# Kernel optimization log

Measured on AMD Instinct MI355X. Metric: run time of the kernel, lower is better.

The kernel has to match this reference:

```python
import jax, jax.numpy as jnp
import numpy as np

N_NODES = 50000
IN_F = 256
OUT_F = 128
N_EDGES = 800000

def setup_inputs() -> dict:
    key = jax.random.key(0)
    k1, k2, k3, k4, k5 = jax.random.split(key, 5)
    x = jax.random.normal(k1, (N_NODES, IN_F), dtype=jnp.float32)
    # xavier_uniform on [in, out]
    limit = float(np.sqrt(6.0 / (IN_F + OUT_F)))
    weight = jax.random.uniform(k2, (IN_F, OUT_F), dtype=jnp.float32, minval=-limit, maxval=limit)
    adj_vals = jax.random.uniform(k3, (N_EDGES,), dtype=jnp.float32)
    adj_rows = jax.random.randint(k4, (N_EDGES,), 0, N_NODES, dtype=jnp.int32)
    adj_cols = jax.random.randint(k5, (N_EDGES,), 0, N_NODES, dtype=jnp.int32)
    return {"x": x, "weight": weight, "adj_vals": adj_vals, "adj_rows": adj_rows, "adj_cols": adj_cols}

def reference(x, weight, adj_vals, adj_rows, adj_cols):
    # dropout p=0.0 (eval) is identity
    support = x @ weight                      # [N, out]
    msgs = adj_vals[:, None] * support[adj_cols]  # [E, out] gather + scale
    output = jax.ops.segment_sum(msgs, adj_rows, num_segments=N_NODES)  # spmm
    return jax.nn.relu(output)
```

## Files before the change

### kernel.cpp

```cpp
#include <hip/hip_runtime.h>
#include <hip/hip_bf16.h>


#define IN_F  256
#define OUT_F 128
#define NPART 8

#define BM 64
#define BK 32
#define KP 40

typedef __attribute__((ext_vector_type(8))) short s16x8;
typedef __attribute__((ext_vector_type(4))) float f32x4;

static __device__ __forceinline__ unsigned short f2bf(float f) {
    union { float f; unsigned u; } v; v.f = f;
    unsigned r = v.u + 0x7FFFu + ((v.u >> 16) & 1u);
    return (unsigned short)(r >> 16);
}
static __device__ __forceinline__ float bf2f(unsigned short b) {
    union { unsigned u; float f; } v; v.u = ((unsigned)b) << 16;
    return v.f;
}

__global__ __launch_bounds__(256) void gcn_wsplit_kernel(
    const float* __restrict__ w, unsigned short* __restrict__ wh_T,
    unsigned short* __restrict__ wl_T)
{
    int cell = blockIdx.x * 256 + threadIdx.x;
    int c  = cell & (OUT_F - 1);
    int kq = cell >> 7;
    unsigned short h[4], l[4];
#pragma unroll
    for (int d = 0; d < 4; ++d) {
        float f = w[(size_t)(kq * 4 + d) * OUT_F + c];
        h[d] = f2bf(f);
        l[d] = f2bf(f - bf2f(h[d]));
    }
    *reinterpret_cast<ushort4*>(&wh_T[(size_t)c * IN_F + kq * 4]) =
        make_ushort4(h[0], h[1], h[2], h[3]);
    *reinterpret_cast<ushort4*>(&wl_T[(size_t)c * IN_F + kq * 4]) =
        make_ushort4(l[0], l[1], l[2], l[3]);
}

__global__ __launch_bounds__(256) void gcn_gemm_mfma_kernel(
    const float* __restrict__ x,
    const unsigned short* __restrict__ wh_T,
    const unsigned short* __restrict__ wl_T,
    unsigned short* __restrict__ support_bf, int n_nodes)
{
    __shared__ unsigned short xh_lds[BM][KP];
    __shared__ unsigned short xl_lds[BM][KP];
    __shared__ unsigned short wh_lds[OUT_F][KP];
    __shared__ unsigned short wl_lds[OUT_F][KP];

    const int tid  = threadIdx.x;
    const int lane = tid & 63;
    const int wid  = tid >> 6;
    const int wm   = (wid >> 1) * 32;
    const int wn   = (wid & 1) * 64;
    const int row0 = blockIdx.x * BM;

    const int lr = lane & 15;
    const int lg = lane >> 4;

    f32x4 acc[2][4];
#pragma unroll
    for (int st = 0; st < 2; ++st)
#pragma unroll
        for (int nt = 0; nt < 4; ++nt)
            acc[st][nt] = (f32x4){0.f, 0.f, 0.f, 0.f};

    for (int k0 = 0; k0 < IN_F; k0 += BK) {
        if (k0 > 0) __syncthreads();

#pragma unroll
        for (int i = 0; i < 2; ++i) {
            int cell = i * 256 + tid;
            int r    = cell >> 3;
            int kq   = cell & 7;
            int row  = row0 + r;
            float4 xv = make_float4(0.f, 0.f, 0.f, 0.f);
            if (row < n_nodes)
                xv = *reinterpret_cast<const float4*>(
                    &x[(size_t)row * IN_F + k0 + kq * 4]);
            unsigned short h0 = f2bf(xv.x), h1 = f2bf(xv.y),
                           h2 = f2bf(xv.z), h3 = f2bf(xv.w);
            *reinterpret_cast<ushort4*>(&xh_lds[r][kq * 4]) =
                make_ushort4(h0, h1, h2, h3);
            *reinterpret_cast<ushort4*>(&xl_lds[r][kq * 4]) =
                make_ushort4(f2bf(xv.x - bf2f(h0)), f2bf(xv.y - bf2f(h1)),
                             f2bf(xv.z - bf2f(h2)), f2bf(xv.w - bf2f(h3)));
        }
#pragma unroll
        for (int i = 0; i < 2; ++i) {
            int cell = i * 256 + tid;
            int c    = cell >> 2;
            int p    = cell & 3;
            s16x8 hv = *reinterpret_cast<const s16x8*>(
                &wh_T[(size_t)c * IN_F + k0 + p * 8]);
            s16x8 lv = *reinterpret_cast<const s16x8*>(
                &wl_T[(size_t)c * IN_F + k0 + p * 8]);
            *reinterpret_cast<s16x8*>(&wh_lds[c][p * 8]) = hv;
            *reinterpret_cast<s16x8*>(&wl_lds[c][p * 8]) = lv;
        }
        __syncthreads();

        s16x8 ah[2], al[2], bh[4], bl[4];
#pragma unroll
        for (int st = 0; st < 2; ++st) {
            int m = wm + st * 16 + lr;
            ah[st] = *reinterpret_cast<const s16x8*>(&xh_lds[m][lg * 8]);
            al[st] = *reinterpret_cast<const s16x8*>(&xl_lds[m][lg * 8]);
        }
#pragma unroll
        for (int nt = 0; nt < 4; ++nt) {
            int c = wn + nt * 16 + lr;
            bh[nt] = *reinterpret_cast<const s16x8*>(&wh_lds[c][lg * 8]);
            bl[nt] = *reinterpret_cast<const s16x8*>(&wl_lds[c][lg * 8]);
        }

#pragma unroll
        for (int st = 0; st < 2; ++st)
#pragma unroll
            for (int nt = 0; nt < 4; ++nt) {
                acc[st][nt] = __builtin_amdgcn_mfma_f32_16x16x32_bf16(
                    ah[st], bh[nt], acc[st][nt], 0, 0, 0);
                acc[st][nt] = __builtin_amdgcn_mfma_f32_16x16x32_bf16(
                    al[st], bh[nt], acc[st][nt], 0, 0, 0);
                acc[st][nt] = __builtin_amdgcn_mfma_f32_16x16x32_bf16(
                    ah[st], bl[nt], acc[st][nt], 0, 0, 0);
            }
    }

#pragma unroll
    for (int st = 0; st < 2; ++st) {
#pragma unroll
        for (int nt = 0; nt < 4; ++nt) {
#pragma unroll
            for (int r = 0; r < 4; ++r) {
                int m = row0 + wm + st * 16 + lg * 4 + r;
                int n = wn + nt * 16 + lr;
                if (m < n_nodes)
                    support_bf[(size_t)m * OUT_F + n] = f2bf(acc[st][nt][r]);
            }
        }
    }
}

#define VBK 32
#define XPAD 68
__global__ __launch_bounds__(256) void gcn_gemm_valu_kernel(
    const float* __restrict__ x, const float* __restrict__ w,
    float* __restrict__ support, int n_nodes)
{
    __shared__ float xs_t[VBK][XPAD];
    __shared__ float ws_[VBK][OUT_F];

    const int tid  = threadIdx.x;
    const int cg   = tid & 31;
    const int rg   = tid >> 5;
    const int row0 = blockIdx.x * BM;

    float acc[8][4];
#pragma unroll
    for (int i = 0; i < 8; ++i)
#pragma unroll
        for (int j = 0; j < 4; ++j) acc[i][j] = 0.f;

    for (int k0 = 0; k0 < IN_F; k0 += VBK) {
        if (k0 > 0) __syncthreads();
#pragma unroll
        for (int i = 0; i < 2; ++i) {
            int t   = tid + i * 256;
            int r   = t >> 3;
            int kk  = (t & 7) << 2;
            int row = row0 + r;
            float4 v = make_float4(0.f, 0.f, 0.f, 0.f);
            if (row < n_nodes)
                v = *reinterpret_cast<const float4*>(&x[(size_t)row * IN_F + k0 + kk]);
            xs_t[kk + 0][r] = v.x;
            xs_t[kk + 1][r] = v.y;
            xs_t[kk + 2][r] = v.z;
            xs_t[kk + 3][r] = v.w;
        }
#pragma unroll
        for (int i = 0; i < 4; ++i) {
            int fi = tid + i * 256;
            int kk = fi >> 5;
            int cc = (fi & 31) << 2;
            *reinterpret_cast<float4*>(&ws_[kk][cc]) =
                *reinterpret_cast<const float4*>(&w[(size_t)(k0 + kk) * OUT_F + cc]);
        }
        __syncthreads();
#pragma unroll
        for (int kk = 0; kk < VBK; ++kk) {
            float4 a0 = *reinterpret_cast<const float4*>(&xs_t[kk][rg * 4]);
            float4 a1 = *reinterpret_cast<const float4*>(&xs_t[kk][rg * 4 + 32]);
            float4 b  = *reinterpret_cast<const float4*>(&ws_[kk][cg * 4]);
            const float av[8] = {a0.x, a0.y, a0.z, a0.w, a1.x, a1.y, a1.z, a1.w};
            const float bv[4] = {b.x, b.y, b.z, b.w};
#pragma unroll
            for (int i = 0; i < 8; ++i)
#pragma unroll
                for (int j = 0; j < 4; ++j)
                    acc[i][j] += av[i] * bv[j];
        }
    }
#pragma unroll
    for (int i = 0; i < 8; ++i) {
        int row = row0 + rg * 4 + (i & 3) + (i >> 2) * 32;
        if (row < n_nodes) {
            float4 o = make_float4(acc[i][0], acc[i][1], acc[i][2], acc[i][3]);
            *reinterpret_cast<float4*>(&support[(size_t)row * OUT_F + cg * 4]) = o;
        }
    }
}

__global__ __launch_bounds__(256) void gcn_hist_kernel(
    const int* __restrict__ rows, int* __restrict__ deg,
    int n_edges, int node_pp)
{
    int part = blockIdx.x & 7;
    int e = (blockIdx.x >> 3) * 256 + threadIdx.x;
    if (e >= n_edges) return;
    int r = rows[e];
    if (r / node_pp != part) return;
    atomicAdd(&deg[r], 1);
}

__global__ __launch_bounds__(256) void gcn_scan1_kernel(
    const int* __restrict__ deg, int* __restrict__ offsets,
    int* __restrict__ block_sums, int n)
{
    __shared__ int part[256];
    const int tid  = threadIdx.x;
    const int base = blockIdx.x * 2048 + tid * 8;

    int v[8];
#pragma unroll
    for (int q = 0; q < 8; ++q) v[q] = 0;
    if (base + 7 < n) {
        int4 a = *reinterpret_cast<const int4*>(&deg[base]);
        int4 b = *reinterpret_cast<const int4*>(&deg[base + 4]);
        v[0] = a.x; v[1] = a.y; v[2] = a.z; v[3] = a.w;
        v[4] = b.x; v[5] = b.y; v[6] = b.z; v[7] = b.w;
    } else {
#pragma unroll
        for (int q = 0; q < 8; ++q)
            if (base + q < n) v[q] = deg[base + q];
    }
    int s = 0;
#pragma unroll
    for (int q = 0; q < 8; ++q) s += v[q];
    part[tid] = s;
    __syncthreads();
    for (int d = 1; d < 256; d <<= 1) {
        int t = (tid >= d) ? part[tid - d] : 0;
        __syncthreads();
        part[tid] += t;
        __syncthreads();
    }
    int run = part[tid] - s;
    int o[8];
#pragma unroll
    for (int q = 0; q < 8; ++q) { o[q] = run; run += v[q]; }
    if (base + 7 < n) {
        *reinterpret_cast<int4*>(&offsets[base])     = make_int4(o[0], o[1], o[2], o[3]);
        *reinterpret_cast<int4*>(&offsets[base + 4]) = make_int4(o[4], o[5], o[6], o[7]);
    } else {
#pragma unroll
        for (int q = 0; q < 8; ++q)
            if (base + q < n) offsets[base + q] = o[q];
    }
    if (tid == 255) block_sums[blockIdx.x] = part[255];
}

__global__ __launch_bounds__(256) void gcn_scan2_kernel(
    int* __restrict__ block_sums, int nb)
{
    __shared__ int part[256];
    const int tid = threadIdx.x;
    int s = (tid < nb) ? block_sums[tid] : 0;
    part[tid] = s;
    __syncthreads();
    for (int d = 1; d < 256; d <<= 1) {
        int t = (tid >= d) ? part[tid - d] : 0;
        __syncthreads();
        part[tid] += t;
        __syncthreads();
    }
    if (tid < nb) block_sums[tid] = part[tid] - s;
}

__global__ __launch_bounds__(256) void gcn_scan3_kernel(
    int* __restrict__ offsets, const int* __restrict__ block_sums, int n)
{
    const int base = blockIdx.x * 2048 + threadIdx.x * 8;
    const int add  = block_sums[blockIdx.x];
    if (base + 7 < n) {
        int4 a = *reinterpret_cast<const int4*>(&offsets[base]);
        int4 b = *reinterpret_cast<const int4*>(&offsets[base + 4]);
        a.x += add; a.y += add; a.z += add; a.w += add;
        b.x += add; b.y += add; b.z += add; b.w += add;
        *reinterpret_cast<int4*>(&offsets[base])     = a;
        *reinterpret_cast<int4*>(&offsets[base + 4]) = b;
    } else {
#pragma unroll
        for (int q = 0; q < 8; ++q)
            if (base + q < n) offsets[base + q] += add;
    }
}

__global__ __launch_bounds__(256) void gcn_fill_kernel(
    const int* __restrict__ rows, const int* __restrict__ cols,
    const float* __restrict__ vals, int* __restrict__ offsets,
    unsigned int* __restrict__ csr_cv, int n_edges, int node_pp)
{
    int part = blockIdx.x & 7;
    int e = (blockIdx.x >> 3) * 256 + threadIdx.x;
    if (e >= n_edges) return;
    int r = rows[e];
    if (r / node_pp != part) return;
    int pos = atomicAdd(&offsets[r], 1);
    unsigned int cv = ((unsigned int)f2bf(vals[e]) << 16) | (unsigned int)cols[e];
    csr_cv[pos] = cv;
}

__global__ __launch_bounds__(256) void gcn_gather_kernel(
    const unsigned short* __restrict__ support_bf,
    const int* __restrict__ offsets,
    const unsigned int* __restrict__ csr_cv,
    float* __restrict__ out, int n_nodes)
{
    const int node = blockIdx.x * 4 + (threadIdx.x >> 6);
    const int lane = threadIdx.x & 63;
    if (node >= n_nodes) return;

    const int end   = offsets[node];
    const int start = (node == 0) ? 0 : offsets[node - 1];

    float2 acc = make_float2(0.f, 0.f);
    int j = start;
    for (; j + 7 < end; j += 8) {
        unsigned int cv[8];
        ushort2 s[8];
#pragma unroll
        for (int q = 0; q < 8; ++q) cv[q] = csr_cv[j + q];
#pragma unroll
        for (int q = 0; q < 8; ++q)
            s[q] = *reinterpret_cast<const ushort2*>(
                &support_bf[(size_t)(cv[q] & 0xFFFFu) * OUT_F + lane * 2]);
#pragma unroll
        for (int q = 0; q < 8; ++q) {
            float v = bf2f((unsigned short)(cv[q] >> 16));
            acc.x += v * bf2f(s[q].x);
            acc.y += v * bf2f(s[q].y);
        }
    }
    for (; j + 1 < end; j += 2) {
        unsigned int cv0 = csr_cv[j];
        unsigned int cv1 = csr_cv[j + 1];
        ushort2 s0 = *reinterpret_cast<const ushort2*>(
            &support_bf[(size_t)(cv0 & 0xFFFFu) * OUT_F + lane * 2]);
        ushort2 s1 = *reinterpret_cast<const ushort2*>(
            &support_bf[(size_t)(cv1 & 0xFFFFu) * OUT_F + lane * 2]);
        float v0 = bf2f((unsigned short)(cv0 >> 16));
        float v1 = bf2f((unsigned short)(cv1 >> 16));
        acc.x += v0 * bf2f(s0.x) + v1 * bf2f(s1.x);
        acc.y += v0 * bf2f(s0.y) + v1 * bf2f(s1.y);
    }
    if (j < end) {
        unsigned int cv0 = csr_cv[j];
        ushort2 s0 = *reinterpret_cast<const ushort2*>(
            &support_bf[(size_t)(cv0 & 0xFFFFu) * OUT_F + lane * 2]);
        float v0 = bf2f((unsigned short)(cv0 >> 16));
        acc.x += v0 * bf2f(s0.x);
        acc.y += v0 * bf2f(s0.y);
    }

    float2 o;
    o.x = fmaxf(acc.x, 0.f);
    o.y = fmaxf(acc.y, 0.f);
    *reinterpret_cast<float2*>(&out[(size_t)node * OUT_F + lane * 2]) = o;
}

__global__ __launch_bounds__(256) void gcn_scatter_kernel(
    const float* __restrict__ support, const float* __restrict__ vals,
    const int* __restrict__ rows, const int* __restrict__ cols,
    float* __restrict__ out, int n_edges)
{
    long long idx   = (long long)blockIdx.x * blockDim.x + threadIdx.x;
    long long total = (long long)n_edges * (OUT_F / 4);
    if (idx >= total) return;

    int e  = (int)(idx >> 5);
    int f4 = (int)(idx & 31);
    int r  = rows[e];
    int c  = cols[e];
    float v = vals[e];

    float4 s = *reinterpret_cast<const float4*>(&support[(size_t)c * OUT_F + f4 * 4]);
    float* o = &out[(size_t)r * OUT_F + f4 * 4];
    atomicAdd(o + 0, v * s.x);
    atomicAdd(o + 1, v * s.y);
    atomicAdd(o + 2, v * s.z);
    atomicAdd(o + 3, v * s.w);
}

__global__ __launch_bounds__(256) void gcn_relu_kernel(float* __restrict__ out, int n4)
{
    int idx = blockIdx.x * blockDim.x + threadIdx.x;
    if (idx >= n4) return;
    float4* p = reinterpret_cast<float4*>(out) + idx;
    float4 v = *p;
    v.x = fmaxf(v.x, 0.f);
    v.y = fmaxf(v.y, 0.f);
    v.z = fmaxf(v.z, 0.f);
    v.w = fmaxf(v.w, 0.f);
    *p = v;
}

static inline char* align16(char* p) {
    return (char*)(((uintptr_t)p + 15) & ~(uintptr_t)15);
}

extern "C" void kernel_launch(void* const* d_in, const int* in_sizes, int n_in,
                              void* d_out, int out_size, void* d_ws, size_t ws_size,
                              hipStream_t stream)
{
    const float* x    = (const float*)d_in[0];
    const float* w    = (const float*)d_in[1];
    const float* vals = (const float*)d_in[2];
    const int*   rows = (const int*)d_in[3];
    const int*   cols = (const int*)d_in[4];
    float* out = (float*)d_out;

    const int n_nodes = in_sizes[0] / IN_F;
    const int n_edges = in_sizes[2];

    const int scan_blocks = (n_nodes + 2047) / 2048;
    const int node_pp     = (n_nodes + NPART - 1) / NPART;

    char* p = (char*)d_ws;
    char*           supp_raw = p;                 p = align16(p + (size_t)n_nodes * OUT_F * sizeof(float));
    unsigned short* wh_T    = (unsigned short*)p; p = align16(p + (size_t)OUT_F * IN_F * sizeof(short));
    unsigned short* wl_T    = (unsigned short*)p; p = align16(p + (size_t)OUT_F * IN_F * sizeof(short));
    int*            offsets = (int*)p;            p = align16(p + (size_t)n_nodes * sizeof(int));
    int*            deg     = (int*)p;            p = align16(p + (size_t)n_nodes * sizeof(int));
    int*            bsums   = (int*)p;            p = align16(p + (size_t)256 * sizeof(int));
    unsigned int*   csr_cv  = (unsigned int*)p;   p = align16(p + (size_t)n_edges * sizeof(unsigned int));
    size_t needed = (size_t)(p - (char*)d_ws);

    const int gemm_blocks = (n_nodes + BM - 1) / BM;
    const int eb = (n_edges + 255) / 256;

    if (ws_size >= needed && scan_blocks <= 256 && n_nodes <= 65536) {
        unsigned short* support_bf = (unsigned short*)supp_raw;
        gcn_wsplit_kernel<<<(OUT_F * IN_F / 4) / 256, 256, 0, stream>>>(w, wh_T, wl_T);
        gcn_gemm_mfma_kernel<<<gemm_blocks, 256, 0, stream>>>(x, wh_T, wl_T,
                                                              support_bf, n_nodes);
        hipMemsetAsync(deg, 0, (size_t)n_nodes * sizeof(int), stream);
        gcn_hist_kernel<<<eb * NPART, 256, 0, stream>>>(rows, deg, n_edges, node_pp);
        gcn_scan1_kernel<<<scan_blocks, 256, 0, stream>>>(deg, offsets, bsums, n_nodes);
        gcn_scan2_kernel<<<1, 256, 0, stream>>>(bsums, scan_blocks);
        gcn_scan3_kernel<<<scan_blocks, 256, 0, stream>>>(offsets, bsums, n_nodes);
        gcn_fill_kernel<<<eb * NPART, 256, 0, stream>>>(rows, cols, vals, offsets,
                                                        csr_cv, n_edges, node_pp);
        int gb = (n_nodes + 3) / 4;
        gcn_gather_kernel<<<gb, 256, 0, stream>>>(support_bf, offsets,
                                                  csr_cv, out, n_nodes);
    } else {
        float* support = (float*)supp_raw;
        gcn_gemm_valu_kernel<<<gemm_blocks, 256, 0, stream>>>(x, w, support, n_nodes);
        hipMemsetAsync(d_out, 0, (size_t)out_size * sizeof(float), stream);
        long long total = (long long)n_edges * (OUT_F / 4);
        int sc_blocks = (int)((total + 255) / 256);
        gcn_scatter_kernel<<<sc_blocks, 256, 0, stream>>>(support, vals, rows, cols,
                                                          out, n_edges);
        int n4 = out_size / 4;
        gcn_relu_kernel<<<(n4 + 255) / 256, 256, 0, stream>>>(out, n4);
    }
}
```

Before: 145.2 us.

## Fuse degree histogram into GEMM, merge memset into prep, collapse scan passes

```diff
diff --git a/kernel.cpp b/kernel.cpp
--- a/kernel.cpp
+++ b/kernel.cpp
@@ -23,31 +23,44 @@
     return v.f;
 }
 
-__global__ __launch_bounds__(256) void gcn_wsplit_kernel(
+__global__ __launch_bounds__(256) void gcn_prep_kernel(
     const float* __restrict__ w, unsigned short* __restrict__ wh_T,
-    unsigned short* __restrict__ wl_T)
-{
-    int cell = blockIdx.x * 256 + threadIdx.x;
-    int c  = cell & (OUT_F - 1);
-    int kq = cell >> 7;
-    unsigned short h[4], l[4];
-#pragma unroll
-    for (int d = 0; d < 4; ++d) {
-        float f = w[(size_t)(kq * 4 + d) * OUT_F + c];
-        h[d] = f2bf(f);
-        l[d] = f2bf(f - bf2f(h[d]));
-    }
-    *reinterpret_cast<ushort4*>(&wh_T[(size_t)c * IN_F + kq * 4]) =
-        make_ushort4(h[0], h[1], h[2], h[3]);
-    *reinterpret_cast<ushort4*>(&wl_T[(size_t)c * IN_F + kq * 4]) =
-        make_ushort4(l[0], l[1], l[2], l[3]);
+    unsigned short* __restrict__ wl_T, int* __restrict__ deg, int n_nodes)
+{
+    int gid = blockIdx.x * 256 + threadIdx.x;
+
+    if (gid < OUT_F * IN_F / 4) {
+        int c  = gid & (OUT_F - 1);
+        int kq = gid >> 7;
+        unsigned short h[4], l[4];
+#pragma unroll
+        for (int d = 0; d < 4; ++d) {
+            float f = w[(size_t)(kq * 4 + d) * OUT_F + c];
+            h[d] = f2bf(f);
+            l[d] = f2bf(f - bf2f(h[d]));
+        }
+        *reinterpret_cast<ushort4*>(&wh_T[(size_t)c * IN_F + kq * 4]) =
+            make_ushort4(h[0], h[1], h[2], h[3]);
+        *reinterpret_cast<ushort4*>(&wl_T[(size_t)c * IN_F + kq * 4]) =
+            make_ushort4(l[0], l[1], l[2], l[3]);
+    }
+
+    int base = gid * 4;
+    if (base + 3 < n_nodes) {
+        *reinterpret_cast<int4*>(&deg[base]) = make_int4(0, 0, 0, 0);
+    } else {
+#pragma unroll
+        for (int q = 0; q < 4; ++q)
+            if (base + q < n_nodes) deg[base + q] = 0;
+    }
 }
 
 __global__ __launch_bounds__(256) void gcn_gemm_mfma_kernel(
     const float* __restrict__ x,
     const unsigned short* __restrict__ wh_T,
     const unsigned short* __restrict__ wl_T,
-    unsigned short* __restrict__ support_bf, int n_nodes)
+    unsigned short* __restrict__ support_bf, int n_nodes,
+    const int* __restrict__ rows, int* __restrict__ deg, int n_edges)
 {
     __shared__ unsigned short xh_lds[BM][KP];
     __shared__ unsigned short xl_lds[BM][KP];
@@ -146,6 +159,10 @@
             }
         }
     }
+
+    const int estride = gridDim.x * 256;
+    for (int e = blockIdx.x * 256 + tid; e < n_edges; e += estride)
+        atomicAdd(&deg[rows[e]], 1);
 }
 
 #define VBK 32
@@ -217,18 +234,6 @@
     }
 }
 
-__global__ __launch_bounds__(256) void gcn_hist_kernel(
-    const int* __restrict__ rows, int* __restrict__ deg,
-    int n_edges, int node_pp)
-{
-    int part = blockIdx.x & 7;
-    int e = (blockIdx.x >> 3) * 256 + threadIdx.x;
-    if (e >= n_edges) return;
-    int r = rows[e];
-    if (r / node_pp != part) return;
-    atomicAdd(&deg[r], 1);
-}
-
 __global__ __launch_bounds__(256) void gcn_scan1_kernel(
     const int* __restrict__ deg, int* __restrict__ offsets,
     int* __restrict__ block_sums, int n)
@@ -276,28 +281,23 @@
     if (tid == 255) block_sums[blockIdx.x] = part[255];
 }
 
-__global__ __launch_bounds__(256) void gcn_scan2_kernel(
-    int* __restrict__ block_sums, int nb)
-{
-    __shared__ int part[256];
+__global__ __launch_bounds__(256) void gcn_scan3_kernel(
+    int* __restrict__ offsets, const int* __restrict__ block_sums,
+    int n, int nb)
+{
+    __shared__ int tmp[256];
     const int tid = threadIdx.x;
-    int s = (tid < nb) ? block_sums[tid] : 0;
-    part[tid] = s;
+    int v = (tid < nb && tid < (int)blockIdx.x) ? block_sums[tid] : 0;
+    tmp[tid] = v;
     __syncthreads();
-    for (int d = 1; d < 256; d <<= 1) {
-        int t = (tid >= d) ? part[tid - d] : 0;
+#pragma unroll
+    for (int d = 128; d > 0; d >>= 1) {
+        if (tid < d) tmp[tid] += tmp[tid + d];
         __syncthreads();
-        part[tid] += t;
-        __syncthreads();
-    }
-    if (tid < nb) block_sums[tid] = part[tid] - s;
-}
-
-__global__ __launch_bounds__(256) void gcn_scan3_kernel(
-    int* __restrict__ offsets, const int* __restrict__ block_sums, int n)
-{
-    const int base = blockIdx.x * 2048 + threadIdx.x * 8;
-    const int add  = block_sums[blockIdx.x];
+    }
+    const int add = tmp[0];
+
+    const int base = blockIdx.x * 2048 + tid * 8;
     if (base + 7 < n) {
         int4 a = *reinterpret_cast<const int4*>(&offsets[base]);
         int4 b = *reinterpret_cast<const int4*>(&offsets[base + 4]);
@@ -457,16 +457,21 @@
 
     if (ws_size >= needed && scan_blocks <= 256 && n_nodes <= 65536) {
         unsigned short* support_bf = (unsigned short*)supp_raw;
-        gcn_wsplit_kernel<<<(OUT_F * IN_F / 4) / 256, 256, 0, stream>>>(w, wh_T, wl_T);
-        gcn_gemm_mfma_kernel<<<gemm_blocks, 256, 0, stream>>>(x, wh_T, wl_T,
-                                                              support_bf, n_nodes);
-        hipMemsetAsync(deg, 0, (size_t)n_nodes * sizeof(int), stream);
-        gcn_hist_kernel<<<eb * NPART, 256, 0, stream>>>(rows, deg, n_edges, node_pp);
+
+        int prep_blocks = max((OUT_F * IN_F / 4 + 255) / 256,
+                              ((n_nodes + 3) / 4 + 255) / 256);
+        gcn_prep_kernel<<<prep_blocks, 256, 0, stream>>>(w, wh_T, wl_T, deg, n_nodes);
+
+        gcn_gemm_mfma_kernel<<<gemm_blocks, 256, 0, stream>>>(
+            x, wh_T, wl_T, support_bf, n_nodes, rows, deg, n_edges);
+
         gcn_scan1_kernel<<<scan_blocks, 256, 0, stream>>>(deg, offsets, bsums, n_nodes);
-        gcn_scan2_kernel<<<1, 256, 0, stream>>>(bsums, scan_blocks);
-        gcn_scan3_kernel<<<scan_blocks, 256, 0, stream>>>(offsets, bsums, n_nodes);
+        gcn_scan3_kernel<<<scan_blocks, 256, 0, stream>>>(offsets, bsums,
+                                                          n_nodes, scan_blocks);
+
         gcn_fill_kernel<<<eb * NPART, 256, 0, stream>>>(rows, cols, vals, offsets,
                                                         csr_cv, n_edges, node_pp);
+
         int gb = (n_nodes + 3) / 4;
         gcn_gather_kernel<<<gb, 256, 0, stream>>>(support_bf, offsets,
                                                   csr_cv, out, n_nodes);
```

Result: faster. 137.6 us (-5.2%).
